# Performance work log

Measured on AMD Instinct MI355X. Metric: run time of the kernel, lower is better.

The kernel has to match this reference:

```python
import jax, jax.numpy as jnp
import numpy as np

B, S, D, V = 8, 128, 1024, 32000
TEMP, TOP_K, TOP_P = 1.0, 50, 0.95
NEG_INF = jnp.float32(-jnp.inf)


def setup_inputs() -> dict:
    key = jax.random.key(0)
    k1, k2, k3, k4 = jax.random.split(key, 4)
    return {
        "psi_real": jax.random.normal(k1, (B, S, D), dtype=jnp.float32),
        "psi_imag": jax.random.normal(k2, (B, S, D), dtype=jnp.float32),
        "W_r": jax.random.normal(k3, (V, D), dtype=jnp.float32) * (1.0 / np.sqrt(D)),
        "W_i": jax.random.normal(k4, (V, D), dtype=jnp.float32) * (1.0 / np.sqrt(D)),
        "bias": jnp.zeros((V,), dtype=jnp.float32),
    }


def reference(psi_real, psi_imag, W_r, W_i, bias):
    # Complex projection: (psi_r + i psi_i) @ (W_r + i W_i)^T
    amp_r = jnp.einsum("bsd,vd->bsv", psi_real, W_r) - jnp.einsum("bsd,vd->bsv", psi_imag, W_i)
    amp_i = jnp.einsum("bsd,vd->bsv", psi_imag, W_r) + jnp.einsum("bsd,vd->bsv", psi_real, W_i)
    amp_sq = amp_r * amp_r + amp_i * amp_i  # Born rule |amp|^2, [B,S,V]
    floor = jnp.mean(amp_sq, axis=-1, keepdims=True) * 1e-6 + 1e-30
    logits = (jnp.log(amp_sq + floor) + bias) / max(TEMP, 1e-8)
    log_probs = jax.nn.log_softmax(logits, axis=-1)

    # top-k filter: keep values >= k-th largest
    kth = jax.lax.top_k(logits, TOP_K)[0][..., -1:]
    filt = jnp.where(logits < kth, NEG_INF, logits)

    # top-p (nucleus) filter on the top-k-filtered logits
    order = jnp.argsort(-filt, axis=-1)                      # descending sort indices
    sorted_logits = jnp.take_along_axis(filt, order, axis=-1)
    sp = jax.nn.softmax(sorted_logits, axis=-1)
    cum = jnp.cumsum(sp, axis=-1)
    drop = (cum - sp) >= TOP_P                               # cumulative prob excluding current token
    sorted_filt = jnp.where(drop, NEG_INF, sorted_logits)
    inv = jnp.argsort(order, axis=-1)                        # scatter back to original order
    filt2 = jnp.take_along_axis(sorted_filt, inv, axis=-1)

    probs = jax.nn.softmax(filt2, axis=-1)
    tokens = jax.random.categorical(jax.random.key(42), filt2, axis=-1)  # multinomial sample [B,S]
    return logits, log_probs, amp_sq, tokens, probs
```

## Files before the change

### kernel.cpp

```cpp
#include <hip/hip_runtime.h>

#define BS   1024
#define DD   1024
#define VV   32000
#define TOPK 50
#define TOPPF 0.95f
#define NVTOT 32768000ull

typedef __attribute__((ext_vector_type(8))) short bf16x8;
typedef __attribute__((ext_vector_type(4))) float f32x4;
typedef __attribute__((ext_vector_type(4))) int   i32x4;

#define MFMA(A,B,C) __builtin_amdgcn_mfma_f32_16x16x32_bf16(A, B, C, 0, 0, 0)

__device__ __forceinline__ unsigned fkey(float f) {
  unsigned u = __float_as_uint(f);
  return (u & 0x80000000u) ? ~u : (u | 0x80000000u);
}
__device__ __forceinline__ unsigned rotl32(unsigned x, int r) {
  return (x << r) | (x >> (32 - r));
}
__device__ __forceinline__ ushort f2bf(float f) {
  unsigned u = __float_as_uint(f);
  unsigned r = ((u >> 16) & 1u) + 0x7FFFu;
  return (ushort)((u + r) >> 16);
}
__device__ __forceinline__ float bf2f(ushort h) {
  return __uint_as_float(((unsigned)h) << 16);
}
__device__ __forceinline__ bf16x8 negbf(bf16x8 a) {
  i32x4 t = __builtin_bit_cast(i32x4, a);
  t = t ^ 0x80008000;
  return __builtin_bit_cast(bf16x8, t);
}

__device__ float gumbel_at(unsigned i) {
  unsigned x0 = 0u, x1 = i;
  const unsigned ks0 = 0u, ks1 = 42u, ks2 = 0x1BD11BDAu ^ 0u ^ 42u;
  x0 += ks0; x1 += ks1;
  const int rotA[4] = {13, 15, 26, 6};
  const int rotB[4] = {17, 29, 16, 24};
#define TF_R4(R) { x0 += x1; x1 = rotl32(x1, R[0]); x1 ^= x0; \
                   x0 += x1; x1 = rotl32(x1, R[1]); x1 ^= x0; \
                   x0 += x1; x1 = rotl32(x1, R[2]); x1 ^= x0; \
                   x0 += x1; x1 = rotl32(x1, R[3]); x1 ^= x0; }
  TF_R4(rotA); x0 += ks1; x1 += ks2 + 1u;
  TF_R4(rotB); x0 += ks2; x1 += ks0 + 2u;
  TF_R4(rotA); x0 += ks0; x1 += ks1 + 3u;
  TF_R4(rotB); x0 += ks1; x1 += ks2 + 4u;
  TF_R4(rotA); x0 += ks2; x1 += ks0 + 5u;
#undef TF_R4
  unsigned bits = x0 ^ x1;
  float f = __uint_as_float(0x3F800000u | (bits >> 9)) - 1.0f;
  float u = fmaxf(f, 1.17549435e-38f);
  return -logf(-logf(u));
}

__global__ __launch_bounds__(256) void pack_split(
    const float* __restrict__ xr, const float* __restrict__ xi,
    ushort* __restrict__ ohr, ushort* __restrict__ olr,
    ushort* __restrict__ ohi, ushort* __restrict__ oli,
    float si, int n4) {
  int g = blockIdx.x * 256 + threadIdx.x;
  if (g >= n4) return;
  int i = g * 4;
  float4 a = *(const float4*)(xr + i);
  float4 b = *(const float4*)(xi + i);
  float av[4] = {a.x, a.y, a.z, a.w};
  float bv[4] = {b.x * si, b.y * si, b.z * si, b.w * si};
  unsigned hr[4], lr[4], hi_[4], li[4];
#pragma unroll
  for (int j = 0; j < 4; ++j) {
    ushort h = f2bf(av[j]);          hr[j] = h;
    lr[j] = f2bf(av[j] - bf2f(h));
    ushort h2 = f2bf(bv[j]);         hi_[j] = h2;
    li[j] = f2bf(bv[j] - bf2f(h2));
  }
  uint2 w;
  w.x = hr[0] | (hr[1] << 16); w.y = hr[2] | (hr[3] << 16);
  *(uint2*)(ohr + i) = w;
  w.x = lr[0] | (lr[1] << 16); w.y = lr[2] | (lr[3] << 16);
  *(uint2*)(olr + i) = w;
  w.x = hi_[0] | (hi_[1] << 16); w.y = hi_[2] | (hi_[3] << 16);
  *(uint2*)(ohi + i) = w;
  w.x = li[0] | (li[1] << 16); w.y = li[2] | (li[3] << 16);
  *(uint2*)(oli + i) = w;
}

__global__ __launch_bounds__(512) void gemm_mfma(
    const ushort* __restrict__ APk,
    const ushort* __restrict__ Wrh, const ushort* __restrict__ Wrl,
    const ushort* __restrict__ Wih, const ushort* __restrict__ Wil,
    float* __restrict__ amp) {
  __shared__ ushort lds[2][8][4096];
  const int tid = threadIdx.x;
  const int lane = tid & 63, wid = tid >> 6;
  const int d = blockIdx.x;
  const int x = d & 7, s = d >> 3;
  const int bm = ((x >> 1) << 1) | (s & 1);
  const int bn = (x & 1) * 125 + (s >> 1);
  const int row0 = bm << 7, col0 = bn << 7;
  const int wm = wid >> 2, wn = wid & 3;

  const ushort* tp[8] = {APk, APk + (1 << 20), APk + (2 << 20), APk + (3 << 20),
                         Wrh, Wrl, Wih, Wil};

  const int rrow = tid >> 2;
  const int ss = (tid & 3) ^ (rrow & 3) ^ ((rrow >> 2) & 3);
  const size_t offA = (size_t)(row0 + rrow) * DD + (ss << 3);
  const size_t offB = (size_t)(col0 + rrow) * DD + (ss << 3);

  f32x4 accr[4][2] = {}, acci[4][2] = {};

  int aoff[4], boff[2];
#pragma unroll
  for (int m = 0; m < 4; ++m) {
    const int ar = (wm << 6) + (m << 4) + (lane & 15);
    aoff[m] = (ar << 6) + ((((lane >> 4)) ^ (ar & 3) ^ ((ar >> 2) & 3)) << 4);
  }
#pragma unroll
  for (int n = 0; n < 2; ++n) {
    const int br = (wn << 5) + (n << 4) + (lane & 15);
    boff[n] = (br << 6) + ((((lane >> 4)) ^ (br & 3) ^ ((br >> 2) & 3)) << 4);
  }

#define STAGE(buf, step) {                                                   \
    const int k0 = (step) << 5;                                              \
    _Pragma("unroll")                                                        \
    for (int t = 0; t < 8; ++t) {                                            \
      const ushort* src = tp[t] + ((t < 4) ? offA : offB) + k0;              \
      __builtin_amdgcn_global_load_lds(                                      \
          (const __attribute__((address_space(1))) unsigned int*)src,        \
          (__attribute__((address_space(3))) unsigned int*)&lds[buf][t][wid << 9], \
          16, 0, 0);                                                         \
    }                                                                        \
  }

  STAGE(0, 0);
  __syncthreads();
  int cur = 0;
  for (int step = 0; step < 32; ++step) {
    if (step + 1 < 32) STAGE(cur ^ 1, step + 1);
    const char* L0 = (const char*)&lds[cur][0][0];
    const char* L1 = (const char*)&lds[cur][1][0];
    const char* L2 = (const char*)&lds[cur][2][0];
    const char* L3 = (const char*)&lds[cur][3][0];
    const char* L4 = (const char*)&lds[cur][4][0];
    const char* L5 = (const char*)&lds[cur][5][0];
    const char* L6 = (const char*)&lds[cur][6][0];
    const char* L7 = (const char*)&lds[cur][7][0];
    bf16x8 aPrh[4], aPrl[4], aNih[4], aNil[4], aPih[4], aPil[4];
#pragma unroll
    for (int m = 0; m < 4; ++m) {
      aPrh[m] = *(const bf16x8*)(L0 + aoff[m]);
      aPrl[m] = *(const bf16x8*)(L1 + aoff[m]);
      aNih[m] = *(const bf16x8*)(L2 + aoff[m]);
      aNil[m] = *(const bf16x8*)(L3 + aoff[m]);
      aPih[m] = negbf(aNih[m]);
      aPil[m] = negbf(aNil[m]);
    }
#pragma unroll
    for (int n = 0; n < 2; ++n) {
      bf16x8 bRh = *(const bf16x8*)(L4 + boff[n]);
      bf16x8 bRl = *(const bf16x8*)(L5 + boff[n]);
      bf16x8 bIh = *(const bf16x8*)(L6 + boff[n]);
      bf16x8 bIl = *(const bf16x8*)(L7 + boff[n]);
#pragma unroll
      for (int m = 0; m < 4; ++m) {
        f32x4 r = accr[m][n], q = acci[m][n];
        r = MFMA(aPrh[m], bRh, r); r = MFMA(aPrh[m], bRl, r); r = MFMA(aPrl[m], bRh, r);
        r = MFMA(aNih[m], bIh, r); r = MFMA(aNih[m], bIl, r); r = MFMA(aNil[m], bIh, r);
        q = MFMA(aPih[m], bRh, q); q = MFMA(aPih[m], bRl, q); q = MFMA(aPil[m], bRh, q);
        q = MFMA(aPrh[m], bIh, q); q = MFMA(aPrh[m], bIl, q); q = MFMA(aPrl[m], bIh, q);
        accr[m][n] = r; acci[m][n] = q;
      }
    }
    __syncthreads();
    cur ^= 1;
  }
#undef STAGE
#pragma unroll
  for (int m = 0; m < 4; ++m)
#pragma unroll
    for (int n = 0; n < 2; ++n)
#pragma unroll
      for (int qi = 0; qi < 4; ++qi) {
        const int row = row0 + (wm << 6) + (m << 4) + ((lane >> 4) << 2) + qi;
        const int col = col0 + (wn << 5) + (n << 4) + (lane & 15);
        float vr = accr[m][n][qi], vi = acci[m][n][qi];
        amp[(size_t)row * VV + col] = vr * vr + vi * vi;
      }
}

__global__ __launch_bounds__(512) void post_row(
    const float* __restrict__ amp, const float* __restrict__ bias,
    float* __restrict__ logits, float* __restrict__ logprobs,
    float* __restrict__ probs, float* __restrict__ tokens) {
  __shared__ __align__(16) float lg[VV];
  __shared__ int hist[4096];
  __shared__ int iscan[512];
  __shared__ float red[512];
  __shared__ float sval[768]; __shared__ int sidx[768];
  __shared__ float ssv[768];  __shared__ int ssi[768];
  __shared__ int scnt;
  __shared__ float sh_f[4];
  __shared__ int   sh_i[4];

  const int row = blockIdx.x, tid = threadIdx.x;
  const float* A = amp + (size_t)row * VV;
  float* Lg = logits + (size_t)row * VV;
  float* Lp = logprobs + (size_t)row * VV;
  float* P  = probs + (size_t)row * VV;

  float s = 0.f;
  for (int i = tid; i < VV / 4; i += 512) {
    float4 a = ((const float4*)A)[i];
    ((float4*)lg)[i] = a;
    s += a.x + a.y + a.z + a.w;
  }
  red[tid] = s; __syncthreads();
  for (int o = 256; o > 0; o >>= 1) { if (tid < o) red[tid] += red[tid + o]; __syncthreads(); }
  if (tid == 0) sh_f[0] = red[0] * (1.0f / (float)VV) * 1e-6f + 1e-30f;
  __syncthreads();
  const float floorv = sh_f[0];
  __syncthreads();

  float mx = -INFINITY;
  for (int i = tid; i < VV / 4; i += 512) {
    float4 a = ((float4*)lg)[i];
    float4 b = ((const float4*)bias)[i];
    float4 l;
    l.x = logf(a.x + floorv) + b.x;
    l.y = logf(a.y + floorv) + b.y;
    l.z = logf(a.z + floorv) + b.z;
    l.w = logf(a.w + floorv) + b.w;
    ((float4*)lg)[i] = l;
    ((float4*)Lg)[i] = l;
    mx = fmaxf(mx, fmaxf(fmaxf(l.x, l.y), fmaxf(l.z, l.w)));
  }
  red[tid] = mx; __syncthreads();
  for (int o = 256; o > 0; o >>= 1) { if (tid < o) red[tid] = fmaxf(red[tid], red[tid + o]); __syncthreads(); }
  mx = red[0]; __syncthreads();

  float se = 0.f;
  for (int i = tid; i < VV / 4; i += 512) {
    float4 l = ((float4*)lg)[i];
    se += expf(l.x - mx) + expf(l.y - mx) + expf(l.z - mx) + expf(l.w - mx);
  }
  red[tid] = se; __syncthreads();
  for (int o = 256; o > 0; o >>= 1) { if (tid < o) red[tid] += red[tid + o]; __syncthreads(); }
  const float lse = mx + logf(red[0]);
  __syncthreads();

  for (int i = tid; i < VV / 4; i += 512) {
    float4 l = ((float4*)lg)[i];
    float4 o4 = {l.x - lse, l.y - lse, l.z - lse, l.w - lse};
    ((float4*)Lp)[i] = o4;
  }

  for (int i = tid; i < 4096; i += 512) hist[i] = 0;
  if (tid == 0) scnt = 0;
  __syncthreads();
  for (int v = tid; v < VV; v += 512)
    atomicAdd(&hist[fkey(lg[v]) >> 20], 1);
  __syncthreads();
  {
    const int hi = 4095 - 8 * tid;
    int part = 0;
#pragma unroll
    for (int j = 0; j < 8; ++j) part += hist[hi - j];
    iscan[tid] = part;
    __syncthreads();
    for (int off = 1; off < 512; off <<= 1) {
      int add = (tid >= off) ? iscan[tid - off] : 0;
      __syncthreads();
      iscan[tid] += add;
      __syncthreads();
    }
    int cum = iscan[tid], prev = tid ? iscan[tid - 1] : 0;
    if (cum >= TOPK && prev < TOPK) sh_i[0] = tid;
    __syncthreads();
    if (tid == 0) {
      int tc = sh_i[0];
      int c = tc ? iscan[tc - 1] : 0;
      int b = 4095 - 8 * tc;
      for (int j = 0; j < 8; ++j) {
        int h = hist[4095 - 8 * tc - j];
        if (c + h >= TOPK) { b = 4095 - 8 * tc - j; break; }
        c += h;
      }
      sh_i[1] = b;
    }
    __syncthreads();
  }
  const unsigned binb = (unsigned)sh_i[1];

  for (int v = tid; v < VV; v += 512) {
    if ((fkey(lg[v]) >> 20) >= binb) {
      int p = atomicAdd(&scnt, 1);
      if (p < 768) { sval[p] = lg[v]; sidx[p] = v; }
    }
  }
  __syncthreads();
  const int n = min(scnt, 768);
  for (int i = tid; i < n; i += 512) {
    float vi = sval[i]; int ii = sidx[i]; int r = 0;
    for (int j = 0; j < n; ++j) {
      float vj = sval[j]; int ij = sidx[j];
      r += (vj > vi) || (vj == vi && ij < ii);
    }
    ssv[r] = vi; ssi[r] = ii;
  }
  __syncthreads();
  if (tid == 0) {
    const float kthv = ssv[TOPK - 1];
    int np = TOPK;
    while (np < n && ssv[np] >= kthv) ++np;
    const float mx2 = ssv[0];
    float denom = 0.f;
    for (int j = 0; j < np; ++j) denom += expf(ssv[j] - mx2);
    float cum = 0.f; int m = np;
    for (int j = 0; j < np; ++j) {
      float sp = expf(ssv[j] - mx2) / denom;
      cum += sp;
      if (cum - sp >= TOPPF) { m = j; break; }
    }
    float dk = 0.f;
    for (int j = 0; j < m; ++j) dk += expf(ssv[j] - mx2);
    sh_f[1] = mx2; sh_f[2] = dk; sh_f[3] = ssv[m - 1];
    sh_i[2] = ssi[m - 1];
  }
  __syncthreads();
  const float mx2 = sh_f[1], dk = sh_f[2], vb = sh_f[3];
  const int ib = sh_i[2];

  float best = -INFINITY; int bidx = 0x7FFFFFFF;
  for (int i = tid; i < VV / 4; i += 512) {
    float4 l4 = ((float4*)lg)[i];
    float lv[4] = {l4.x, l4.y, l4.z, l4.w};
    float4 p4 = {0.f, 0.f, 0.f, 0.f};
    float pv[4] = {0.f, 0.f, 0.f, 0.f};
#pragma unroll
    for (int j = 0; j < 4; ++j) {
      const int v = i * 4 + j;
      float l = lv[j];
      bool kept = (l > vb) || (l == vb && v <= ib);
      if (kept) {
        pv[j] = expf(l - mx2) / dk;
        float g = gumbel_at((unsigned)(row * VV + v));
        float sc = l + g;
        if (sc > best || (sc == best && v < bidx)) { best = sc; bidx = v; }
      }
    }
    p4.x = pv[0]; p4.y = pv[1]; p4.z = pv[2]; p4.w = pv[3];
    ((float4*)P)[i] = p4;
  }
  red[tid] = best; iscan[tid] = bidx; __syncthreads();
  for (int o = 256; o > 0; o >>= 1) {
    if (tid < o) {
      if (red[tid + o] > red[tid] ||
          (red[tid + o] == red[tid] && iscan[tid + o] < iscan[tid])) {
        red[tid] = red[tid + o]; iscan[tid] = iscan[tid + o];
      }
    }
    __syncthreads();
  }
  if (tid == 0) tokens[row] = (float)iscan[0];
}

extern "C" void kernel_launch(void* const* d_in, const int* in_sizes, int n_in,
                              void* d_out, int out_size, void* d_ws, size_t ws_size,
                              hipStream_t stream) {
  const float* pr   = (const float*)d_in[0];
  const float* pi   = (const float*)d_in[1];
  const float* wr   = (const float*)d_in[2];
  const float* wi   = (const float*)d_in[3];
  const float* bias = (const float*)d_in[4];

  float* out      = (float*)d_out;
  float* logits   = out;
  float* logprobs = out + NVTOT;
  float* ampsq    = out + 2 * NVTOT;
  float* tokens   = out + 3 * NVTOT;
  float* probs    = out + 3 * NVTOT + 1024;

  ushort* Wrh = (ushort*)logits;
  ushort* Wrl = Wrh + 32768000;
  ushort* Wih = (ushort*)logprobs;
  ushort* Wil = Wih + 32768000;
  ushort* APk = (ushort*)probs;

  pack_split<<<1024, 256, 0, stream>>>(pr, pi,
      APk, APk + (1 << 20), APk + (2 << 20), APk + (3 << 20), -1.0f, 262144);
  pack_split<<<32000, 256, 0, stream>>>(wr, wi,
      Wrh, Wrl, Wih, Wil, 1.0f, 8192000);

  gemm_mfma<<<2000, 512, 0, stream>>>(APk, Wrh, Wrl, Wih, Wil, ampsq);

  post_row<<<BS, 512, 0, stream>>>(ampsq, bias, logits, logprobs, probs, tokens);
}
```

Before: 1.0000 ms.

## Widen post_row to 1024 threads, use wave-shuffle reductions, fuse logprob write

The per-row postprocessing kernel moves from 512 to 1024 threads. Its shared-memory tree reductions become wavefront shuffle reductions followed by a 16-entry cross-wave pass. The separate pass that wrote log-probs is merged into the final probability and sampling pass, which saves one sweep over the shared logits and several barriers. The larger block raises register pressure, and the histogram scan now leaves half the threads idle.

```diff
diff --git a/kernel.cpp b/kernel.cpp
--- a/kernel.cpp
+++ b/kernel.cpp
@@ -192,14 +192,13 @@
       }
 }
 
-__global__ __launch_bounds__(512) void post_row(
+__global__ __launch_bounds__(1024) void post_row(
     const float* __restrict__ amp, const float* __restrict__ bias,
     float* __restrict__ logits, float* __restrict__ logprobs,
     float* __restrict__ probs, float* __restrict__ tokens) {
   __shared__ __align__(16) float lg[VV];
   __shared__ int hist[4096];
   __shared__ int iscan[512];
-  __shared__ float red[512];
   __shared__ float sval[768]; __shared__ int sidx[768];
   __shared__ float ssv[768];  __shared__ int ssi[768];
   __shared__ int scnt;
@@ -207,26 +206,34 @@
   __shared__ int   sh_i[4];
 
   const int row = blockIdx.x, tid = threadIdx.x;
+  const int lane = tid & 63, wv = tid >> 6;
   const float* A = amp + (size_t)row * VV;
   float* Lg = logits + (size_t)row * VV;
   float* Lp = logprobs + (size_t)row * VV;
   float* P  = probs + (size_t)row * VV;
+  float* redf = (float*)hist;
 
   float s = 0.f;
-  for (int i = tid; i < VV / 4; i += 512) {
+  for (int i = tid; i < VV / 4; i += 1024) {
     float4 a = ((const float4*)A)[i];
     ((float4*)lg)[i] = a;
     s += a.x + a.y + a.z + a.w;
   }
-  red[tid] = s; __syncthreads();
-  for (int o = 256; o > 0; o >>= 1) { if (tid < o) red[tid] += red[tid + o]; __syncthreads(); }
-  if (tid == 0) sh_f[0] = red[0] * (1.0f / (float)VV) * 1e-6f + 1e-30f;
+#pragma unroll
+  for (int o = 32; o > 0; o >>= 1) s += __shfl_down(s, o, 64);
+  if (lane == 0) redf[wv] = s;
+  __syncthreads();
+  if (tid == 0) {
+    float t = 0.f;
+    for (int j = 0; j < 16; ++j) t += redf[j];
+    sh_f[0] = t * (1.0f / (float)VV) * 1e-6f + 1e-30f;
+  }
   __syncthreads();
   const float floorv = sh_f[0];
   __syncthreads();
 
   float mx = -INFINITY;
-  for (int i = tid; i < VV / 4; i += 512) {
+  for (int i = tid; i < VV / 4; i += 1024) {
     float4 a = ((float4*)lg)[i];
     float4 b = ((const float4*)bias)[i];
     float4 l;
@@ -238,47 +245,62 @@
     ((float4*)Lg)[i] = l;
     mx = fmaxf(mx, fmaxf(fmaxf(l.x, l.y), fmaxf(l.z, l.w)));
   }
-  red[tid] = mx; __syncthreads();
-  for (int o = 256; o > 0; o >>= 1) { if (tid < o) red[tid] = fmaxf(red[tid], red[tid + o]); __syncthreads(); }
-  mx = red[0]; __syncthreads();
+#pragma unroll
+  for (int o = 32; o > 0; o >>= 1) mx = fmaxf(mx, __shfl_down(mx, o, 64));
+  if (lane == 0) redf[wv] = mx;
+  __syncthreads();
+  if (tid == 0) {
+    float t = -INFINITY;
+    for (int j = 0; j < 16; ++j) t = fmaxf(t, redf[j]);
+    sh_f[0] = t;
+  }
+  __syncthreads();
+  mx = sh_f[0];
+  __syncthreads();
 
   float se = 0.f;
-  for (int i = tid; i < VV / 4; i += 512) {
+  for (int i = tid; i < VV / 4; i += 1024) {
     float4 l = ((float4*)lg)[i];
     se += expf(l.x - mx) + expf(l.y - mx) + expf(l.z - mx) + expf(l.w - mx);
   }
-  red[tid] = se; __syncthreads();
-  for (int o = 256; o > 0; o >>= 1) { if (tid < o) red[tid] += red[tid + o]; __syncthreads(); }
-  const float lse = mx + logf(red[0]);
-  __syncthreads();
-
-  for (int i = tid; i < VV / 4; i += 512) {
-    float4 l = ((float4*)lg)[i];
-    float4 o4 = {l.x - lse, l.y - lse, l.z - lse, l.w - lse};
-    ((float4*)Lp)[i] = o4;
-  }
-
-  for (int i = tid; i < 4096; i += 512) hist[i] = 0;
+#pragma unroll
+  for (int o = 32; o > 0; o >>= 1) se += __shfl_down(se, o, 64);
+  if (lane == 0) redf[wv] = se;
+  __syncthreads();
+  if (tid == 0) {
+    float t = 0.f;
+    for (int j = 0; j < 16; ++j) t += redf[j];
+    sh_f[0] = mx + logf(t);
+  }
+  __syncthreads();
+  const float lse = sh_f[0];
+  __syncthreads();
+
+  for (int i = tid; i < 4096; i += 1024) hist[i] = 0;
   if (tid == 0) scnt = 0;
   __syncthreads();
-  for (int v = tid; v < VV; v += 512)
+  for (int v = tid; v < VV; v += 1024)
     atomicAdd(&hist[fkey(lg[v]) >> 20], 1);
   __syncthreads();
   {
-    const int hi = 4095 - 8 * tid;
-    int part = 0;
-#pragma unroll
-    for (int j = 0; j < 8; ++j) part += hist[hi - j];
-    iscan[tid] = part;
+    if (tid < 512) {
+      const int hi = 4095 - 8 * tid;
+      int part = 0;
+#pragma unroll
+      for (int j = 0; j < 8; ++j) part += hist[hi - j];
+      iscan[tid] = part;
+    }
     __syncthreads();
     for (int off = 1; off < 512; off <<= 1) {
-      int add = (tid >= off) ? iscan[tid - off] : 0;
+      int add = (tid < 512 && tid >= off) ? iscan[tid - off] : 0;
       __syncthreads();
-      iscan[tid] += add;
+      if (tid < 512) iscan[tid] += add;
       __syncthreads();
     }
-    int cum = iscan[tid], prev = tid ? iscan[tid - 1] : 0;
-    if (cum >= TOPK && prev < TOPK) sh_i[0] = tid;
+    if (tid < 512) {
+      int cum = iscan[tid], prev = tid ? iscan[tid - 1] : 0;
+      if (cum >= TOPK && prev < TOPK) sh_i[0] = tid;
+    }
     __syncthreads();
     if (tid == 0) {
       int tc = sh_i[0];
@@ -295,7 +317,7 @@
   }
   const unsigned binb = (unsigned)sh_i[1];
 
-  for (int v = tid; v < VV; v += 512) {
+  for (int v = tid; v < VV; v += 1024) {
     if ((fkey(lg[v]) >> 20) >= binb) {
       int p = atomicAdd(&scnt, 1);
       if (p < 768) { sval[p] = lg[v]; sidx[p] = v; }
@@ -303,7 +325,7 @@
   }
   __syncthreads();
   const int n = min(scnt, 768);
-  for (int i = tid; i < n; i += 512) {
+  for (int i = tid; i < n; i += 1024) {
     float vi = sval[i]; int ii = sidx[i]; int r = 0;
     for (int j = 0; j < n; ++j) {
       float vj = sval[j]; int ij = sidx[j];
@@ -335,10 +357,11 @@
   const int ib = sh_i[2];
 
   float best = -INFINITY; int bidx = 0x7FFFFFFF;
-  for (int i = tid; i < VV / 4; i += 512) {
+  for (int i = tid; i < VV / 4; i += 1024) {
     float4 l4 = ((float4*)lg)[i];
     float lv[4] = {l4.x, l4.y, l4.z, l4.w};
-    float4 p4 = {0.f, 0.f, 0.f, 0.f};
+    float4 o4 = {l4.x - lse, l4.y - lse, l4.z - lse, l4.w - lse};
+    ((float4*)Lp)[i] = o4;
     float pv[4] = {0.f, 0.f, 0.f, 0.f};
 #pragma unroll
     for (int j = 0; j < 4; ++j) {
@@ -352,20 +375,28 @@
         if (sc > best || (sc == best && v < bidx)) { best = sc; bidx = v; }
       }
     }
-    p4.x = pv[0]; p4.y = pv[1]; p4.z = pv[2]; p4.w = pv[3];
+    float4 p4 = {pv[0], pv[1], pv[2], pv[3]};
     ((float4*)P)[i] = p4;
   }
-  red[tid] = best; iscan[tid] = bidx; __syncthreads();
-  for (int o = 256; o > 0; o >>= 1) {
-    if (tid < o) {
-      if (red[tid + o] > red[tid] ||
-          (red[tid + o] == red[tid] && iscan[tid + o] < iscan[tid])) {
-        red[tid] = red[tid + o]; iscan[tid] = iscan[tid + o];
+#pragma unroll
+  for (int o = 32; o > 0; o >>= 1) {
+    float ov = __shfl_down(best, o, 64);
+    int   oi = __shfl_down(bidx, o, 64);
+    if (ov > best || (ov == best && oi < bidx)) { best = ov; bidx = oi; }
+  }
+  {
+    float* wv_v = (float*)hist;
+    int*   wv_i = hist + 16;
+    if (lane == 0) { wv_v[wv] = best; wv_i[wv] = bidx; }
+    __syncthreads();
+    if (tid == 0) {
+      float bv = -INFINITY; int bi = 0x7FFFFFFF;
+      for (int j = 0; j < 16; ++j) {
+        if (wv_v[j] > bv || (wv_v[j] == bv && wv_i[j] < bi)) { bv = wv_v[j]; bi = wv_i[j]; }
       }
-    }
-    __syncthreads();
-  }
-  if (tid == 0) tokens[row] = (float)iscan[0];
+      tokens[row] = (float)bi;
+    }
+  }
 }
 
 extern "C" void kernel_launch(void* const* d_in, const int* in_sizes, int n_in,
@@ -397,5 +428,5 @@
 
   gemm_mfma<<<2000, 512, 0, stream>>>(APk, Wrh, Wrl, Wih, Wil, ampsq);
 
-  post_row<<<BS, 512, 0, stream>>>(ampsq, bias, logits, logprobs, probs, tokens);
-}
+  post_row<<<BS, 1024, 0, stream>>>(ampsq, bias, logits, logprobs, probs, tokens);
+}
```

New measurement: 935.1 us. 1.07x faster.
